# Performance work log

Measured on AMD Instinct MI355X. Metric: run time of the kernel, lower is better.

Reference implementation:

```python
import jax, jax.numpy as jnp
import numpy as np

# ---- static config (matches init_kwargs) ----
WS = 7            # window_size
SHIFT = 3         # shift_size (SW-MSA block)
Z, X, Y = 14, 28, 56
DIM = 384
HEADS = 12
HD = DIM // HEADS
N = WS ** 3       # tokens per 3D window = 343
SCALE = HD ** (-0.5)
TBL = (2 * WS - 1) ** 3
B = 2
L = Z * X * Y
NW = (Z // WS) * (X // WS) * (Y // WS)  # 64 windows
MLP_H = 4 * DIM


def _rel_index():
    # Faithful to source: only coords 0 and 1 are offset, coord 0 scaled by (2*Wx-1).
    c = np.stack(np.meshgrid(np.arange(WS), np.arange(WS), np.arange(WS), indexing='ij')).reshape(3, -1)
    r = (c[:, :, None] - c[:, None, :]).transpose(1, 2, 0).astype(np.int64)
    r[..., 0] += WS - 1
    r[..., 1] += WS - 1
    r[..., 0] *= 2 * WS - 1
    idx = r.sum(-1)
    return np.mod(idx, TBL)  # torch wraps negative indices; mod reproduces that

REL_IDX = jnp.asarray(_rel_index())  # (N, N)


def _attn_mask():
    img = np.zeros((1, Z, X, Y, 1))
    sl = (slice(0, -WS), slice(-WS, -SHIFT), slice(-SHIFT, None))
    cnt = 0
    for a in sl:
        for b in sl:
            for c in sl:
                img[:, a, b, c, :] = cnt
                cnt += 1
    w = img.reshape(1, Z // WS, WS, X // WS, WS, Y // WS, WS, 1)
    w = w.transpose(0, 1, 3, 5, 2, 4, 6, 7).reshape(-1, N)
    d = w[:, None, :] - w[:, :, None]
    return np.where(d != 0, -100.0, 0.0).astype(np.float32)  # (NW, N, N)

ATTN_MASK = jnp.asarray(_attn_mask())


def _ln(x, g, b):
    m = x.mean(-1, keepdims=True)
    v = jnp.mean(jnp.square(x - m), axis=-1, keepdims=True)
    return (x - m) * jax.lax.rsqrt(v + 1e-5) * g + b


def _window_partition(x):  # (B,Z,X,Y,C) -> (B*NW, N, C)
    x = x.reshape(B, Z // WS, WS, X // WS, WS, Y // WS, WS, DIM)
    x = x.transpose(0, 1, 3, 5, 2, 4, 6, 7)
    return x.reshape(-1, N, DIM)


def _window_reverse(w):  # (B*NW, N, C) -> (B,Z,X,Y,C)
    x = w.reshape(B, Z // WS, X // WS, Y // WS, WS, WS, WS, DIM)
    x = x.transpose(0, 1, 4, 2, 5, 3, 6, 7)
    return x.reshape(B, Z, X, Y, DIM)


def setup_inputs() -> dict:
    key = jax.random.key(0)
    ks = jax.random.split(key, 8)
    f32 = jnp.float32
    p = {}
    p['x'] = jax.random.normal(ks[0], (B, L, DIM), f32)
    p['norm1_g'] = jnp.ones((DIM,), f32)
    p['norm1_b'] = jnp.zeros((DIM,), f32)
    p['qkv_w'] = (jax.random.normal(ks[1], (DIM, 3 * DIM), f32) * 0.02)
    p['qkv_b'] = jnp.zeros((3 * DIM,), f32)
    p['proj_w'] = (jax.random.normal(ks[2], (DIM, DIM), f32) * 0.02)
    p['proj_b'] = jnp.zeros((DIM,), f32)
    p['rel_tbl'] = (jax.random.normal(ks[3], (TBL, HEADS), f32) * 0.02)
    p['norm2_g'] = jnp.ones((DIM,), f32)
    p['norm2_b'] = jnp.zeros((DIM,), f32)
    p['fc1_w'] = (jax.random.normal(ks[4], (DIM, MLP_H), f32) * 0.02)
    p['fc1_b'] = jnp.zeros((MLP_H,), f32)
    p['fc2_w'] = (jax.random.normal(ks[5], (MLP_H, DIM), f32) * 0.02)
    p['fc2_b'] = jnp.zeros((DIM,), f32)
    return p


def reference(x, norm1_g, norm1_b, qkv_w, qkv_b, proj_w, proj_b, rel_tbl,
              norm2_g, norm2_b, fc1_w, fc1_b, fc2_w, fc2_b):
    shortcut = x
    h = _ln(x, norm1_g, norm1_b).reshape(B, Z, X, Y, DIM)
    # cyclic shift
    h = jnp.roll(h, (-SHIFT, -SHIFT, -SHIFT), axis=(1, 2, 3))
    w = _window_partition(h)                       # (B*NW, N, C)
    qkv = (w @ qkv_w + qkv_b).reshape(-1, N, 3, HEADS, HD).transpose(2, 0, 3, 1, 4)
    q, k, v = qkv[0] * SCALE, qkv[1], qkv[2]       # (B*NW, H, N, hd)
    attn = jnp.einsum('bhnd,bhmd->bhnm', q, k)
    bias = rel_tbl[REL_IDX].transpose(2, 0, 1)     # (H, N, N)
    attn = attn + bias[None]
    attn = attn.reshape(B, NW, HEADS, N, N) + ATTN_MASK[None, :, None]
    attn = jax.nn.softmax(attn.reshape(-1, HEADS, N, N), axis=-1)
    o = jnp.einsum('bhnm,bhmd->bhnd', attn, v).transpose(0, 2, 1, 3).reshape(-1, N, DIM)
    o = o @ proj_w + proj_b
    h = _window_reverse(o)
    h = jnp.roll(h, (SHIFT, SHIFT, SHIFT), axis=(1, 2, 3)).reshape(B, L, DIM)
    x = shortcut + h
    m = _ln(x, norm2_g, norm2_b)
    m = jax.nn.gelu(m @ fc1_w + fc1_b, approximate=False) @ fc2_w + fc2_b
    return x + m
```

## Files before the change

### kernel.cpp

```cpp
#include <hip/hip_runtime.h>
#include <hip/hip_bf16.h>
#include <cmath>

typedef float f32x4 __attribute__((ext_vector_type(4)));
typedef float f32x16 __attribute__((ext_vector_type(16)));
typedef short bf16x8 __attribute__((ext_vector_type(8)));
typedef const __attribute__((address_space(1))) unsigned int* gas_t;
typedef __attribute__((address_space(3))) unsigned int* las_t;

#define GLOAD16(g, l) __builtin_amdgcn_global_load_lds((gas_t)(const void*)(g), (las_t)(void*)(l), 16, 0, 0)

#define LOG2E 1.4426950408889634f
#define MASKC (-144.2695040888963f)
#define SL2E  (0.17677669529663687f * 1.4426950408889634f)

static __device__ __forceinline__ float bf2f(unsigned short u){
  return __uint_as_float(((unsigned)u) << 16);
}
static __device__ __forceinline__ unsigned short f2bf(float f){
  unsigned u = __float_as_uint(f);
  unsigned r = u + 0x7FFFu + ((u >> 16) & 1u);
  return (unsigned short)(r >> 16);
}
static __device__ __forceinline__ unsigned packbf(float a, float b){
  union { __hip_bfloat162 h; unsigned u; } cv;
  cv.h = __float22bfloat162_rn(make_float2(a, b));
  return cv.u;
}
static __device__ __forceinline__ f32x16 zero16(){
  f32x16 z;
  #pragma unroll
  for (int i = 0; i < 16; i++) z[i] = 0.f;
  return z;
}

__global__ __launch_bounds__(256) void padzero_kernel(unsigned short* __restrict__ qs2,
                                                      unsigned short* __restrict__ ks2,
                                                      unsigned short* __restrict__ vt2){
  const int wh = blockIdx.x;
  uint4 z = make_uint4(0, 0, 0, 0);
  const size_t base = (size_t)wh * 11264 + 10 * 1024;
  for (int i = threadIdx.x; i < 384; i += 256){
    int arr = i >> 7, slot = i & 127;
    unsigned short* p = (arr == 0 ? qs2 : (arr == 1 ? ks2 : vt2));
    *(uint4*)(p + base + slot * 8) = z;
  }
}

__global__ __launch_bounds__(256) void wconv2_kernel(const float* __restrict__ in,
                                                     unsigned short* __restrict__ out,
                                                     int K, int N){
  __shared__ unsigned short t[32][33];
  int tx = threadIdx.x & 31, ty = threadIdx.x >> 5;
  int n0 = blockIdx.x * 32, k0 = blockIdx.y * 32;
  #pragma unroll
  for (int i = 0; i < 4; i++)
    t[ty + 8 * i][tx] = f2bf(in[(size_t)(k0 + ty + 8 * i) * N + n0 + tx]);
  __syncthreads();
  #pragma unroll
  for (int i = 0; i < 4; i++)
    out[(size_t)(n0 + ty + 8 * i) * K + k0 + tx] = t[tx][ty + 8 * i];
}

__global__ void biasprep_kernel(const float* __restrict__ rel, unsigned short* __restrict__ bias12){
  int p = blockIdx.x * 256 + threadIdx.x;
  if (p >= 743424) return;
  int h = p / 61952;
  int rem = p - h * 61952;
  int q = rem / 176;
  int m2 = (rem - q * 176) * 2;
  int qi0 = q / 49, qr = q - qi0 * 49, qi1 = qr / 7, qi2 = qr - qi1 * 7;
  unsigned v[2];
  #pragma unroll
  for (int j = 0; j < 2; j++){
    int m = m2 + j;
    float val;
    if (m >= 343) val = -1.4426950e30f;
    else {
      int mi0 = m / 49, mr = m - mi0 * 49, mi1 = mr / 7, mi2 = mr - mi1 * 7;
      int idx = 13 * (qi0 - mi0 + 6) + (qi1 - mi1 + 6) + (qi2 - mi2);
      if (idx < 0) idx += 2197;
      val = rel[idx * 12 + h] * LOG2E;
    }
    v[j] = f2bf(val);
  }
  *(unsigned*)(&bias12[(size_t)h * 123904 + q * 352 + m2]) = v[0] | (v[1] << 16);
}

__global__ void maskprep_kernel(unsigned* __restrict__ bitmapG){
  int id = blockIdx.x * 256 + threadIdx.x;
  if (id >= 8 * 352) return;
  int cls = id / 352, q = id - cls * 352;
  int qi0 = q / 49, qr = q - qi0 * 49, qi1 = qr / 7, qi2 = qr - qi1 * 7;
  int az = (cls & 4) ? (qi0 < 4 ? 1 : 2) : 0;
  int ax = (cls & 2) ? (qi1 < 4 ? 1 : 2) : 0;
  int ay = (cls & 1) ? (qi2 < 4 ? 1 : 2) : 0;
  int cq = az * 9 + ax * 3 + ay;
  unsigned w[11];
  #pragma unroll
  for (int t = 0; t < 11; t++) w[t] = 0u;
  for (int m = 0; m < 352; m++){
    int mi0 = m / 49, mr = m - mi0 * 49, mi1 = mr / 7, mi2 = mr - mi1 * 7;
    int bz = (cls & 4) ? (mi0 < 4 ? 1 : 2) : 0;
    int bx = (cls & 2) ? (mi1 < 4 ? 1 : 2) : 0;
    int by = (cls & 1) ? (mi2 < 4 ? 1 : 2) : 0;
    if (bz * 9 + bx * 3 + by != cq) w[m >> 5] |= (1u << (m & 31));
  }
  unsigned* dst = bitmapG + (size_t)id * 12;
  #pragma unroll
  for (int t = 0; t < 11; t++) dst[t] = w[t];
  dst[11] = 0u;
}

template<int MODE>
__global__ __launch_bounds__(256) void ln_kernel(const float* __restrict__ in,
                                                 const float* __restrict__ g,
                                                 const float* __restrict__ bta,
                                                 unsigned short* __restrict__ out){
  int wave = threadIdx.x >> 6, lane = threadIdx.x & 63;
  int row = blockIdx.x * 4 + wave;
  size_t srow;
  if (MODE == 0){
    int win = row / 343, n = row - win * 343;
    int b = win >> 6, w64 = win & 63;
    int zw = w64 >> 5, xw = (w64 >> 3) & 3, yw = w64 & 7;
    int i0 = n / 49, nr = n - i0 * 49, i1 = nr / 7, i2 = nr - i1 * 7;
    int zs = zw * 7 + i0 + 3; if (zs >= 14) zs -= 14;
    int xs = xw * 7 + i1 + 3; if (xs >= 28) xs -= 28;
    int ys = yw * 7 + i2 + 3; if (ys >= 56) ys -= 56;
    srow = (size_t)b * 21952 + zs * 1568 + xs * 56 + ys;
  } else {
    srow = (size_t)row;
  }
  const float* p = in + srow * 384;
  float v[6]; float s = 0.f;
  #pragma unroll
  for (int i = 0; i < 6; i++){ v[i] = p[lane + i * 64]; s += v[i]; }
  #pragma unroll
  for (int off = 32; off >= 1; off >>= 1) s += __shfl_xor(s, off);
  float mean = s * (1.f / 384.f);
  float vs = 0.f;
  #pragma unroll
  for (int i = 0; i < 6; i++){ float d = v[i] - mean; vs += d * d; }
  #pragma unroll
  for (int off = 32; off >= 1; off >>= 1) vs += __shfl_xor(vs, off);
  float rstd = rsqrtf(vs * (1.f / 384.f) + 1e-5f);
  unsigned short* o = out + (size_t)row * 384;
  #pragma unroll
  for (int i = 0; i < 6; i++){
    int c = lane + i * 64;
    o[c] = f2bf((v[i] - mean) * rstd * g[c] + bta[c]);
  }
}

template<int EPI>
__global__ __launch_bounds__(256, 4) void gemm2(
    const unsigned short* __restrict__ A,
    const unsigned short* __restrict__ Bt,
    const float* __restrict__ bias,
    const float* __restrict__ resid,
    void* __restrict__ outp,
    unsigned short* __restrict__ oq,
    unsigned short* __restrict__ ok,
    unsigned short* __restrict__ ov,
    int K, int ldc, int nt_){
  __shared__ unsigned short As[8192];
  __shared__ unsigned short Bs[8192];
  const int nwg = gridDim.x;
  const int qq = nwg >> 3, rr = nwg & 7;
  const int xcd = blockIdx.x & 7, pos = blockIdx.x >> 3;
  const int wgid = (xcd < rr ? xcd * (qq + 1) : rr * (qq + 1) + (xcd - rr) * qq) + pos;
  const int mtile = wgid / nt_, ntile = wgid - mtile * nt_;
  const int r0 = mtile * 128, c0 = ntile * 128;

  const int tid = threadIdx.x, lane = tid & 63, wave = tid >> 6;
  const int wr = (wave >> 1) * 64, wc = (wave & 1) * 64;
  f32x4 acc[4][4];
  #pragma unroll
  for (int mi = 0; mi < 4; mi++)
    #pragma unroll
    for (int ni = 0; ni < 4; ni++) acc[mi][ni] = f32x4{0.f, 0.f, 0.f, 0.f};

  const int srow = lane >> 2;
  const int koff = ((lane & 3) ^ ((lane >> 3) & 3)) * 8;
  const int kkey = (lane >> 1) & 3;

  for (int k0 = 0; k0 < K; k0 += 64){
    __syncthreads();
    #pragma unroll
    for (int i = 0; i < 8; i++){
      const int id = wave + i * 4;
      const int arr = id >> 4;
      const int within = id & 15;
      const int ksub = within >> 3;
      const int sub = within & 7;
      const unsigned short* g = (arr ? Bt : A)
          + (size_t)((arr ? c0 : r0) + sub * 16 + srow) * K + k0 + ksub * 32 + koff;
      unsigned short* dst = (arr ? Bs : As) + ksub * 4096 + sub * 512;
      GLOAD16(g, dst);
    }
    __syncthreads();
    #pragma unroll
    for (int ks = 0; ks < 2; ks++){
      bf16x8 af[4], bfr[4];
      #pragma unroll
      for (int mi = 0; mi < 4; mi++)
        af[mi] = *(const bf16x8*)(&As[ks * 4096 + (wr + mi * 16 + (lane & 15)) * 32 + (((lane >> 4) ^ kkey) * 8)]);
      #pragma unroll
      for (int ni = 0; ni < 4; ni++)
        bfr[ni] = *(const bf16x8*)(&Bs[ks * 4096 + (wc + ni * 16 + (lane & 15)) * 32 + (((lane >> 4) ^ kkey) * 8)]);
      #pragma unroll
      for (int mi = 0; mi < 4; mi++)
        #pragma unroll
        for (int ni = 0; ni < 4; ni++)
          acc[mi][ni] = __builtin_amdgcn_mfma_f32_16x16x32_bf16(bfr[ni], af[mi], acc[mi][ni], 0, 0, 0);
    }
  }

  const int lrow = lane & 15;
  const int cq4  = (lane >> 4) << 2;
  #pragma unroll
  for (int mi = 0; mi < 4; mi++){
    const int row = r0 + wr + mi * 16 + lrow;
    int win, m, t, mloc, vh2;
    size_t sdst;
    if (EPI == 0 || EPI == 1){ win = row / 343; m = row - win * 343; }
    if (EPI == 0){
      t = m >> 5; mloc = m & 31;
      vh2 = ((m >> 4) & 1) * 512 + ((m >> 3) & 1) * 256 + (m & 7);
    }
    if (EPI == 1){
      const int b = win >> 6, w64 = win & 63;
      const int zw = w64 >> 5, xw = (w64 >> 3) & 3, yw = w64 & 7;
      const int i0 = m / 49, nr = m - i0 * 49, i1 = nr / 7, i2 = nr - i1 * 7;
      int zf = zw * 7 + i0 + 3; if (zf >= 14) zf -= 14;
      int xf = xw * 7 + i1 + 3; if (xf >= 28) xf -= 28;
      int yf = yw * 7 + i2 + 3; if (yf >= 56) yf -= 56;
      sdst = ((size_t)b * 21952 + zf * 1568 + xf * 56 + yf) * 384;
    }
    #pragma unroll
    for (int ni = 0; ni < 4; ni++){
      const int colb = c0 + wc + ni * 16 + cq4;
      float v[4];
      #pragma unroll
      for (int j = 0; j < 4; j++) v[j] = acc[mi][ni][j] + bias[colb + j];
      if (EPI == 2){
        #pragma unroll
        for (int j = 0; j < 4; j++)
          v[j] = v[j] * __builtin_amdgcn_rcpf(1.0f + exp2f(v[j] * -2.4554669f));
        uint2 st; st.x = packbf(v[0], v[1]); st.y = packbf(v[2], v[3]);
        *(uint2*)((unsigned short*)outp + (size_t)row * ldc + colb) = st;
      } else if (EPI == 3){
        const float* rsd = resid + (size_t)row * ldc + colb;
        f32x4 q = *(const f32x4*)rsd;
        f32x4 o4; o4[0] = v[0] + q[0]; o4[1] = v[1] + q[1];
        o4[2] = v[2] + q[2]; o4[3] = v[3] + q[3];
        *(f32x4*)((float*)outp + (size_t)row * ldc + colb) = o4;
      } else if (EPI == 1){
        const float* rsd = resid + sdst + colb;
        f32x4 q = *(const f32x4*)rsd;
        f32x4 o4; o4[0] = v[0] + q[0]; o4[1] = v[1] + q[1];
        o4[2] = v[2] + q[2]; o4[3] = v[3] + q[3];
        *(f32x4*)((float*)outp + sdst + colb) = o4;
      } else {
        if (c0 < 384){
          #pragma unroll
          for (int j = 0; j < 4; j++) v[j] *= SL2E;
          const int d = colb, h = d >> 5, dd = d & 31;
          const size_t off = (size_t)(win * 12 + h) * 11264
              + (size_t)(t * 1024 + ((dd >> 4) & 1) * 512 + ((dd >> 3) & 1) * 256 + mloc * 8 + (dd & 7));
          uint2 st; st.x = packbf(v[0], v[1]); st.y = packbf(v[2], v[3]);
          *(uint2*)(oq + off) = st;
        } else if (c0 < 768){
          const int d = colb - 384, h = d >> 5, dd = d & 31;
          const size_t off = (size_t)(win * 12 + h) * 11264
              + (size_t)(t * 1024 + ((dd >> 4) & 1) * 512 + ((dd >> 3) & 1) * 256 + mloc * 8 + (dd & 7));
          uint2 st; st.x = packbf(v[0], v[1]); st.y = packbf(v[2], v[3]);
          *(uint2*)(ok + off) = st;
        } else {
          const int d = colb - 768, h = d >> 5, dd = d & 31;
          const size_t off = (size_t)(win * 12 + h) * 11264 + (size_t)(t * 1024 + vh2);
          #pragma unroll
          for (int j = 0; j < 4; j++)
            ov[off + (size_t)(dd + j) * 8] = f2bf(v[j]);
        }
      }
    }
  }
}

__global__ __launch_bounds__(256, 4) void attn3_kernel(
    const unsigned short* __restrict__ qs2,
    const unsigned short* __restrict__ ks2,
    const unsigned short* __restrict__ vt2,
    const unsigned short* __restrict__ bias12,
    const unsigned* __restrict__ bitmapG,
    unsigned short* __restrict__ out){
  __shared__ unsigned short Ks[11264];
  __shared__ unsigned short Ps[4][1280];
  const int wh = blockIdx.x;
  const int win = wh / 12, h = wh - win * 12;
  const int tid = threadIdx.x, wave = tid >> 6, lane = tid & 63;
  const int ln = lane & 31, hh = lane >> 5;

  const unsigned short* ksrc = ks2 + (size_t)wh * 11264;
  for (int c = wave; c < 22; c += 4)
    GLOAD16(ksrc + c * 512 + lane * 8, &Ks[c * 512]);

  const int w64 = win & 63;
  const int cls = ((((w64 >> 5) & 1) == 1 ? 4 : 0)) | ((((w64 >> 3) & 3) == 3) ? 2 : 0) | (((w64 & 7) == 7) ? 1 : 0);
  __syncthreads();

  const unsigned short* qbase = qs2 + (size_t)wh * 11264;
  const unsigned short* vbase = vt2 + (size_t)wh * 11264;

  for (int qt = wave; qt < 11; qt += 4){
    const int q_lane = qt * 32 + ln;
    const bf16x8 bq0 = *(const bf16x8*)(qbase + qt * 1024 + hh * 256 + ln * 8);
    const bf16x8 bq1 = *(const bf16x8*)(qbase + qt * 1024 + 512 + hh * 256 + ln * 8);
    const unsigned short* brow = bias12 + ((size_t)h * 352 + q_lane) * 352;
    const unsigned* mrow = bitmapG + (size_t)(cls * 352 + q_lane) * 12;

    f32x16 o = zero16();
    float sum = 0.f;
    bf16x8 nbv0 = *(const bf16x8*)(vbase + hh * 256 + ln * 8);
    bf16x8 nbv1 = *(const bf16x8*)(vbase + 512 + hh * 256 + ln * 8);
    ushort4 nb0 = *(const ushort4*)(brow + hh * 4);
    ushort4 nb1 = *(const ushort4*)(brow + 8 + hh * 4);
    ushort4 nb2 = *(const ushort4*)(brow + 16 + hh * 4);
    ushort4 nb3 = *(const ushort4*)(brow + 24 + hh * 4);
    unsigned nwm = mrow[0];

    for (int t = 0; t < 11; t++){
      const bf16x8 bv0 = nbv0, bv1 = nbv1;
      const ushort4 cb0 = nb0, cb1 = nb1, cb2 = nb2, cb3 = nb3;
      const unsigned wm = nwm;
      if (t < 10){
        const unsigned short* vnext = vbase + (t + 1) * 1024;
        nbv0 = *(const bf16x8*)(vnext + hh * 256 + ln * 8);
        nbv1 = *(const bf16x8*)(vnext + 512 + hh * 256 + ln * 8);
        const unsigned short* bnext = brow + (t + 1) * 32;
        nb0 = *(const ushort4*)(bnext + hh * 4);
        nb1 = *(const ushort4*)(bnext + 8 + hh * 4);
        nb2 = *(const ushort4*)(bnext + 16 + hh * 4);
        nb3 = *(const ushort4*)(bnext + 24 + hh * 4);
        nwm = mrow[t + 1];
      }
      const bf16x8 ka0 = *(const bf16x8*)(&Ks[t * 1024 + hh * 256 + ln * 8]);
      const bf16x8 ka1 = *(const bf16x8*)(&Ks[t * 1024 + 512 + hh * 256 + ln * 8]);
      f32x16 acc = zero16();
      acc = __builtin_amdgcn_mfma_f32_32x32x16_bf16(ka0, bq0, acc, 0, 0, 0);
      acc = __builtin_amdgcn_mfma_f32_32x32x16_bf16(ka1, bq1, acc, 0, 0, 0);

      const unsigned wsh = wm >> (4 * hh);
      float pv[16];
      unsigned short cbv[16];
      *(ushort4*)(&cbv[0]) = cb0; *(ushort4*)(&cbv[4]) = cb1;
      *(ushort4*)(&cbv[8]) = cb2; *(ushort4*)(&cbv[12]) = cb3;
      #pragma unroll
      for (int g = 0; g < 4; g++){
        #pragma unroll
        for (int i = 0; i < 4; i++){
          const int r = g * 4 + i;
          float s = acc[r] + bf2f(cbv[r]);
          if (cls){
            if (wsh & (1u << (i + 8 * g))) s += MASKC;
          }
          float e = exp2f(s);
          sum += e;
          pv[r] = e;
        }
      }
      #pragma unroll
      for (int g = 0; g < 4; g++){
        uint2 pk;
        pk.x = packbf(pv[4 * g], pv[4 * g + 1]);
        pk.y = packbf(pv[4 * g + 2], pv[4 * g + 3]);
        *(uint2*)(&Ps[wave][ln * 40 + 8 * g + 4 * hh]) = pk;
      }
      const bf16x8 pa0 = *(const bf16x8*)(&Ps[wave][ln * 40 + 8 * hh]);
      const bf16x8 pa1 = *(const bf16x8*)(&Ps[wave][ln * 40 + 16 + 8 * hh]);
      o = __builtin_amdgcn_mfma_f32_32x32x16_bf16(pa0, bv0, o, 0, 0, 0);
      o = __builtin_amdgcn_mfma_f32_32x32x16_bf16(pa1, bv1, o, 0, 0, 0);
    }
    sum += __shfl_xor(sum, 32);
    const float inv = 1.f / sum;
    #pragma unroll
    for (int r = 0; r < 16; r++){
      const int qloc = (r & 3) + 8 * (r >> 2) + 4 * hh;
      const float iv = __shfl(inv, qloc);
      const int qg = qt * 32 + qloc;
      if (qg < 343)
        out[((size_t)win * 343 + qg) * 384 + h * 32 + ln] = f2bf(o[r] * iv);
    }
  }
}

extern "C" void kernel_launch(void* const* d_in, const int* in_sizes, int n_in,
                              void* d_out, int out_size, void* d_ws, size_t ws_size,
                              hipStream_t stream){
  const float* x      = (const float*)d_in[0];
  const float* n1g    = (const float*)d_in[1];
  const float* n1b    = (const float*)d_in[2];
  const float* qkv_w  = (const float*)d_in[3];
  const float* qkv_b  = (const float*)d_in[4];
  const float* proj_w = (const float*)d_in[5];
  const float* proj_b = (const float*)d_in[6];
  const float* rel    = (const float*)d_in[7];
  const float* n2g    = (const float*)d_in[8];
  const float* n2b    = (const float*)d_in[9];
  const float* fc1_w  = (const float*)d_in[10];
  const float* fc1_b  = (const float*)d_in[11];
  const float* fc2_w  = (const float*)d_in[12];
  const float* fc2_b  = (const float*)d_in[13];
  float* out = (float*)d_out;

  char* ws = (char*)d_ws;
  unsigned short* w_win  = (unsigned short*)(ws + 0);
  unsigned short* hidden = (unsigned short*)(ws + 0);
  unsigned short* qs2    = (unsigned short*)(ws + 33718272ull);
  unsigned short* ks2    = (unsigned short*)(ws + 68321280ull);
  unsigned short* vt2    = (unsigned short*)(ws + 102924288ull);
  float*          x2     = (float*)(ws + 134873088ull);
  unsigned short* bias12 = (unsigned short*)(ws + 137527296ull);
  unsigned*       bitmapG= (unsigned*)(ws + 140504064ull);
  unsigned short* att    = (unsigned short*)(ws + 202309632ull);
  unsigned short* ln2    = att;
  unsigned short* wt_qkv = (unsigned short*)(ws + 236027904ull);
  unsigned short* wt_prj = (unsigned short*)(ws + 236912640ull);
  unsigned short* wt_fc1 = (unsigned short*)(ws + 237207552ull);
  unsigned short* wt_fc2 = (unsigned short*)(ws + 238387200ull);

  wconv2_kernel<<<dim3(36, 12), 256, 0, stream>>>(qkv_w, wt_qkv, 384, 1152);
  wconv2_kernel<<<dim3(12, 12), 256, 0, stream>>>(proj_w, wt_prj, 384, 384);
  wconv2_kernel<<<dim3(48, 12), 256, 0, stream>>>(fc1_w, wt_fc1, 384, 1536);
  wconv2_kernel<<<dim3(12, 48), 256, 0, stream>>>(fc2_w, wt_fc2, 1536, 384);
  biasprep_kernel<<<2904, 256, 0, stream>>>(rel, bias12);
  maskprep_kernel<<<11, 256, 0, stream>>>(bitmapG);
  padzero_kernel<<<1536, 256, 0, stream>>>(qs2, ks2, vt2);

  ln_kernel<0><<<10976, 256, 0, stream>>>(x, n1g, n1b, w_win);
  gemm2<0><<<343 * 9, 256, 0, stream>>>(w_win, wt_qkv, qkv_b, nullptr, nullptr,
                                        qs2, ks2, vt2, 384, 0, 9);
  attn3_kernel<<<1536, 256, 0, stream>>>(qs2, ks2, vt2, bias12, bitmapG, att);
  gemm2<1><<<343 * 3, 256, 0, stream>>>(att, wt_prj, proj_b, x, x2,
                                        nullptr, nullptr, nullptr, 384, 384, 3);
  ln_kernel<1><<<10976, 256, 0, stream>>>(x2, n2g, n2b, ln2);
  gemm2<2><<<343 * 12, 256, 0, stream>>>(ln2, wt_fc1, fc1_b, nullptr, hidden,
                                         nullptr, nullptr, nullptr, 384, 1536, 12);
  gemm2<3><<<343 * 3, 256, 0, stream>>>(hidden, wt_fc2, fc2_b, x2, out,
                                        nullptr, nullptr, nullptr, 1536, 384, 3);
}
```

Measured before the change: 504.1 us.

## Precompute fused bias+mask in MFMA fragment layout and use permlane swap for P

A new prep kernel builds a per-(mask class, head) fp32 table of relative-position bias plus shift mask, stored in the exact MFMA accumulator fragment order, and replaces the separate bf16 bias and bitmap-mask tables. The attention kernel then seeds the QK^T accumulator directly from this table, removing per-element bias conversion and mask bit tests. It also replaces the LDS round-trip used to re-layout P for the PV matmul with v_permlane32_swap register shuffles, dropping the per-wave LDS buffer. The cost is a larger fp32 bias table (8 classes × 12 heads) read from global memory in every tile, which adds memory traffic.

Measured after the change: 449.7 us. 1.12x faster.

```diff
diff --git a/kernel.cpp b/kernel.cpp
--- a/kernel.cpp
+++ b/kernel.cpp
@@ -62,54 +62,38 @@
     out[(size_t)(n0 + ty + 8 * i) * K + k0 + tx] = t[tx][ty + 8 * i];
 }
 
-__global__ void biasprep_kernel(const float* __restrict__ rel, unsigned short* __restrict__ bias12){
-  int p = blockIdx.x * 256 + threadIdx.x;
-  if (p >= 743424) return;
-  int h = p / 61952;
-  int rem = p - h * 61952;
-  int q = rem / 176;
-  int m2 = (rem - q * 176) * 2;
-  int qi0 = q / 49, qr = q - qi0 * 49, qi1 = qr / 7, qi2 = qr - qi1 * 7;
-  unsigned v[2];
-  #pragma unroll
-  for (int j = 0; j < 2; j++){
-    int m = m2 + j;
+__global__ __launch_bounds__(256) void biasprep3_kernel(const float* __restrict__ rel,
+                                                        float* __restrict__ biasF){
+  const int plane = blockIdx.y;
+  const int cls = plane / 12, h = plane - cls * 12;
+  const int qt = blockIdx.x / 11, t = blockIdx.x - qt * 11;
+  const int tid = threadIdx.x;
+  const int lane = tid >> 2, rb = (tid & 3) * 4;
+  const int q = qt * 32 + (lane & 31);
+  f32x4 v;
+  #pragma unroll
+  for (int j = 0; j < 4; j++){
+    const int r = rb + j;
+    const int mm = t * 32 + (r & 3) + 8 * (r >> 2) + 4 * (lane >> 5);
     float val;
-    if (m >= 343) val = -1.4426950e30f;
+    if (q >= 343 || mm >= 343) val = -1e30f;
     else {
-      int mi0 = m / 49, mr = m - mi0 * 49, mi1 = mr / 7, mi2 = mr - mi1 * 7;
+      int qi0 = q / 49, qr = q - qi0 * 49, qi1 = qr / 7, qi2 = qr - qi1 * 7;
+      int mi0 = mm / 49, mr = mm - mi0 * 49, mi1 = mr / 7, mi2 = mr - mi1 * 7;
       int idx = 13 * (qi0 - mi0 + 6) + (qi1 - mi1 + 6) + (qi2 - mi2);
       if (idx < 0) idx += 2197;
       val = rel[idx * 12 + h] * LOG2E;
-    }
-    v[j] = f2bf(val);
-  }
-  *(unsigned*)(&bias12[(size_t)h * 123904 + q * 352 + m2]) = v[0] | (v[1] << 16);
-}
-
-__global__ void maskprep_kernel(unsigned* __restrict__ bitmapG){
-  int id = blockIdx.x * 256 + threadIdx.x;
-  if (id >= 8 * 352) return;
-  int cls = id / 352, q = id - cls * 352;
-  int qi0 = q / 49, qr = q - qi0 * 49, qi1 = qr / 7, qi2 = qr - qi1 * 7;
-  int az = (cls & 4) ? (qi0 < 4 ? 1 : 2) : 0;
-  int ax = (cls & 2) ? (qi1 < 4 ? 1 : 2) : 0;
-  int ay = (cls & 1) ? (qi2 < 4 ? 1 : 2) : 0;
-  int cq = az * 9 + ax * 3 + ay;
-  unsigned w[11];
-  #pragma unroll
-  for (int t = 0; t < 11; t++) w[t] = 0u;
-  for (int m = 0; m < 352; m++){
-    int mi0 = m / 49, mr = m - mi0 * 49, mi1 = mr / 7, mi2 = mr - mi1 * 7;
-    int bz = (cls & 4) ? (mi0 < 4 ? 1 : 2) : 0;
-    int bx = (cls & 2) ? (mi1 < 4 ? 1 : 2) : 0;
-    int by = (cls & 1) ? (mi2 < 4 ? 1 : 2) : 0;
-    if (bz * 9 + bx * 3 + by != cq) w[m >> 5] |= (1u << (m & 31));
-  }
-  unsigned* dst = bitmapG + (size_t)id * 12;
-  #pragma unroll
-  for (int t = 0; t < 11; t++) dst[t] = w[t];
-  dst[11] = 0u;
+      int az = (cls & 4) ? (qi0 < 4 ? 1 : 2) : 0;
+      int ax = (cls & 2) ? (qi1 < 4 ? 1 : 2) : 0;
+      int ay = (cls & 1) ? (qi2 < 4 ? 1 : 2) : 0;
+      int bz = (cls & 4) ? (mi0 < 4 ? 1 : 2) : 0;
+      int bx = (cls & 2) ? (mi1 < 4 ? 1 : 2) : 0;
+      int by = (cls & 1) ? (mi2 < 4 ? 1 : 2) : 0;
+      if (az * 9 + ax * 3 + ay != bz * 9 + bx * 3 + by) val += MASKC;
+    }
+    v[j] = val;
+  }
+  *(f32x4*)(biasF + ((size_t)plane * 121 + blockIdx.x) * 1024 + tid * 4) = v;
 }
 
 template<int MODE>
@@ -289,15 +273,13 @@
   }
 }
 
-__global__ __launch_bounds__(256, 4) void attn3_kernel(
+__global__ __launch_bounds__(256, 4) void attn4_kernel(
     const unsigned short* __restrict__ qs2,
     const unsigned short* __restrict__ ks2,
     const unsigned short* __restrict__ vt2,
-    const unsigned short* __restrict__ bias12,
-    const unsigned* __restrict__ bitmapG,
+    const float* __restrict__ biasF,
     unsigned short* __restrict__ out){
   __shared__ unsigned short Ks[11264];
-  __shared__ unsigned short Ps[4][1280];
   const int wh = blockIdx.x;
   const int win = wh / 12, h = wh - win * 12;
   const int tid = threadIdx.x, wave = tid >> 6, lane = tid & 63;
@@ -308,80 +290,58 @@
     GLOAD16(ksrc + c * 512 + lane * 8, &Ks[c * 512]);
 
   const int w64 = win & 63;
-  const int cls = ((((w64 >> 5) & 1) == 1 ? 4 : 0)) | ((((w64 >> 3) & 3) == 3) ? 2 : 0) | (((w64 & 7) == 7) ? 1 : 0);
+  const int cls = (((w64 >> 5) & 1) ? 4 : 0) | ((((w64 >> 3) & 3) == 3) ? 2 : 0) | (((w64 & 7) == 7) ? 1 : 0);
   __syncthreads();
 
   const unsigned short* qbase = qs2 + (size_t)wh * 11264;
   const unsigned short* vbase = vt2 + (size_t)wh * 11264;
+  const float* bbase = biasF + (size_t)(cls * 12 + h) * 123904 + lane * 16;
 
   for (int qt = wave; qt < 11; qt += 4){
-    const int q_lane = qt * 32 + ln;
     const bf16x8 bq0 = *(const bf16x8*)(qbase + qt * 1024 + hh * 256 + ln * 8);
     const bf16x8 bq1 = *(const bf16x8*)(qbase + qt * 1024 + 512 + hh * 256 + ln * 8);
-    const unsigned short* brow = bias12 + ((size_t)h * 352 + q_lane) * 352;
-    const unsigned* mrow = bitmapG + (size_t)(cls * 352 + q_lane) * 12;
+    const float* brow = bbase + (size_t)qt * 11264;
 
     f32x16 o = zero16();
     float sum = 0.f;
     bf16x8 nbv0 = *(const bf16x8*)(vbase + hh * 256 + ln * 8);
     bf16x8 nbv1 = *(const bf16x8*)(vbase + 512 + hh * 256 + ln * 8);
-    ushort4 nb0 = *(const ushort4*)(brow + hh * 4);
-    ushort4 nb1 = *(const ushort4*)(brow + 8 + hh * 4);
-    ushort4 nb2 = *(const ushort4*)(brow + 16 + hh * 4);
-    ushort4 nb3 = *(const ushort4*)(brow + 24 + hh * 4);
-    unsigned nwm = mrow[0];
+    f32x16 nbF = *(const f32x16*)(brow);
 
     for (int t = 0; t < 11; t++){
       const bf16x8 bv0 = nbv0, bv1 = nbv1;
-      const ushort4 cb0 = nb0, cb1 = nb1, cb2 = nb2, cb3 = nb3;
-      const unsigned wm = nwm;
+      f32x16 acc = nbF;
       if (t < 10){
         const unsigned short* vnext = vbase + (t + 1) * 1024;
         nbv0 = *(const bf16x8*)(vnext + hh * 256 + ln * 8);
         nbv1 = *(const bf16x8*)(vnext + 512 + hh * 256 + ln * 8);
-        const unsigned short* bnext = brow + (t + 1) * 32;
-        nb0 = *(const ushort4*)(bnext + hh * 4);
-        nb1 = *(const ushort4*)(bnext + 8 + hh * 4);
-        nb2 = *(const ushort4*)(bnext + 16 + hh * 4);
-        nb3 = *(const ushort4*)(bnext + 24 + hh * 4);
-        nwm = mrow[t + 1];
+        nbF = *(const f32x16*)(brow + (t + 1) * 1024);
       }
       const bf16x8 ka0 = *(const bf16x8*)(&Ks[t * 1024 + hh * 256 + ln * 8]);
       const bf16x8 ka1 = *(const bf16x8*)(&Ks[t * 1024 + 512 + hh * 256 + ln * 8]);
-      f32x16 acc = zero16();
       acc = __builtin_amdgcn_mfma_f32_32x32x16_bf16(ka0, bq0, acc, 0, 0, 0);
       acc = __builtin_amdgcn_mfma_f32_32x32x16_bf16(ka1, bq1, acc, 0, 0, 0);
 
-      const unsigned wsh = wm >> (4 * hh);
       float pv[16];
-      unsigned short cbv[16];
-      *(ushort4*)(&cbv[0]) = cb0; *(ushort4*)(&cbv[4]) = cb1;
-      *(ushort4*)(&cbv[8]) = cb2; *(ushort4*)(&cbv[12]) = cb3;
       #pragma unroll
-      for (int g = 0; g < 4; g++){
-        #pragma unroll
-        for (int i = 0; i < 4; i++){
-          const int r = g * 4 + i;
-          float s = acc[r] + bf2f(cbv[r]);
-          if (cls){
-            if (wsh & (1u << (i + 8 * g))) s += MASKC;
-          }
-          float e = exp2f(s);
-          sum += e;
-          pv[r] = e;
-        }
+      for (int r = 0; r < 16; r++){
+        const float e = exp2f(acc[r]);
+        sum += e;
+        pv[r] = e;
       }
-      #pragma unroll
-      for (int g = 0; g < 4; g++){
-        uint2 pk;
-        pk.x = packbf(pv[4 * g], pv[4 * g + 1]);
-        pk.y = packbf(pv[4 * g + 2], pv[4 * g + 3]);
-        *(uint2*)(&Ps[wave][ln * 40 + 8 * g + 4 * hh]) = pk;
-      }
-      const bf16x8 pa0 = *(const bf16x8*)(&Ps[wave][ln * 40 + 8 * hh]);
-      const bf16x8 pa1 = *(const bf16x8*)(&Ps[wave][ln * 40 + 16 + 8 * hh]);
-      o = __builtin_amdgcn_mfma_f32_32x32x16_bf16(pa0, bv0, o, 0, 0, 0);
-      o = __builtin_amdgcn_mfma_f32_32x32x16_bf16(pa1, bv1, o, 0, 0, 0);
+      unsigned a0 = packbf(pv[0], pv[1]),  b0 = packbf(pv[4], pv[5]);
+      unsigned a1 = packbf(pv[2], pv[3]),  b1 = packbf(pv[6], pv[7]);
+      unsigned a2 = packbf(pv[8], pv[9]),  b2 = packbf(pv[12], pv[13]);
+      unsigned a3 = packbf(pv[10], pv[11]), b3 = packbf(pv[14], pv[15]);
+      asm volatile("v_permlane32_swap_b32 %0, %1" : "+v"(a0), "+v"(b0));
+      asm volatile("v_permlane32_swap_b32 %0, %1" : "+v"(a1), "+v"(b1));
+      asm volatile("v_permlane32_swap_b32 %0, %1" : "+v"(a2), "+v"(b2));
+      asm volatile("v_permlane32_swap_b32 %0, %1" : "+v"(a3), "+v"(b3));
+      union { unsigned u[4]; bf16x8 v; } p0c, p1c;
+      p0c.u[0] = a0; p0c.u[1] = a1; p0c.u[2] = b0; p0c.u[3] = b1;
+      p1c.u[0] = a2; p1c.u[1] = a3; p1c.u[2] = b2; p1c.u[3] = b3;
+      o = __builtin_amdgcn_mfma_f32_32x32x16_bf16(p0c.v, bv0, o, 0, 0, 0);
+      o = __builtin_amdgcn_mfma_f32_32x32x16_bf16(p1c.v, bv1, o, 0, 0, 0);
     }
     sum += __shfl_xor(sum, 32);
     const float inv = 1.f / sum;
@@ -422,8 +382,7 @@
   unsigned short* ks2    = (unsigned short*)(ws + 68321280ull);
   unsigned short* vt2    = (unsigned short*)(ws + 102924288ull);
   float*          x2     = (float*)(ws + 134873088ull);
-  unsigned short* bias12 = (unsigned short*)(ws + 137527296ull);
-  unsigned*       bitmapG= (unsigned*)(ws + 140504064ull);
+  float*          biasF  = (float*)(ws + 137527296ull);
   unsigned short* att    = (unsigned short*)(ws + 202309632ull);
   unsigned short* ln2    = att;
   unsigned short* wt_qkv = (unsigned short*)(ws + 236027904ull);
@@ -435,14 +394,13 @@
   wconv2_kernel<<<dim3(12, 12), 256, 0, stream>>>(proj_w, wt_prj, 384, 384);
   wconv2_kernel<<<dim3(48, 12), 256, 0, stream>>>(fc1_w, wt_fc1, 384, 1536);
   wconv2_kernel<<<dim3(12, 48), 256, 0, stream>>>(fc2_w, wt_fc2, 1536, 384);
-  biasprep_kernel<<<2904, 256, 0, stream>>>(rel, bias12);
-  maskprep_kernel<<<11, 256, 0, stream>>>(bitmapG);
+  biasprep3_kernel<<<dim3(121, 96), 256, 0, stream>>>(rel, biasF);
   padzero_kernel<<<1536, 256, 0, stream>>>(qs2, ks2, vt2);
 
   ln_kernel<0><<<10976, 256, 0, stream>>>(x, n1g, n1b, w_win);
   gemm2<0><<<343 * 9, 256, 0, stream>>>(w_win, wt_qkv, qkv_b, nullptr, nullptr,
                                         qs2, ks2, vt2, 384, 0, 9);
-  attn3_kernel<<<1536, 256, 0, stream>>>(qs2, ks2, vt2, bias12, bitmapG, att);
+  attn4_kernel<<<1536, 256, 0, stream>>>(qs2, ks2, vt2, biasF, att);
   gemm2<1><<<343 * 3, 256, 0, stream>>>(att, wt_prj, proj_b, x, x2,
                                         nullptr, nullptr, nullptr, 384, 384, 3);
   ln_kernel<1><<<10976, 256, 0, stream>>>(x2, n2g, n2b, ln2);
```
